# Kernel tuning notes

Measured on AMD Instinct MI355X. Metric: run time of the kernel, lower is better.

Reference implementation:

```python
import jax, jax.numpy as jnp
from jax import lax
import numpy as np

T, B, D = 1024, 2, 1024
E, TOP_K, ED, HD, MAXP = 12, 4, 256, 64, 64
H = ED // HD  # num_heads = 4


def setup_inputs() -> dict:
    rng = jax.random.key(0)
    ks = jax.random.split(rng, 9)
    s = 0.02
    return {
        "query": jax.random.normal(ks[0], (T, B, D), jnp.float32),
        "key": jax.random.normal(ks[1], (T, B, D), jnp.float32),
        "value": jax.random.normal(ks[2], (T, B, D), jnp.float32),
        "w_gate": jax.random.normal(ks[3], (D, E), jnp.float32) * s,
        "w_map": jax.random.normal(ks[4], (E, D, ED), jnp.float32) * s,
        "w_reduce": jax.random.normal(ks[5], (E, ED, D), jnp.float32) * s,
        "wk": jax.random.normal(ks[6], (D, ED), jnp.float32) * s,
        "wv": jax.random.normal(ks[7], (D, ED), jnp.float32) * s,
        "rel_pos_emb": jax.random.normal(ks[8], (H, HD, 2 * MAXP + 1), jnp.float32) * s,
    }


def reference(query, key, value, w_gate, w_map, w_reduce, wk, wv, rel_pos_emb):
    t, b, d = query.shape
    n = t * b
    scaling = HD ** (-0.25)

    # ---- MoE map (q projection): softmax gating, top-k dispatch ----
    x = query.reshape(n, d)
    probs = jax.nn.softmax(x @ w_gate, axis=-1)          # [N,E]
    gates, idx = lax.top_k(probs, TOP_K)                 # [N,K]
    all_map = jnp.einsum('nd,edh->neh', x, w_map)        # [N,E,ED]
    q = jnp.take_along_axis(all_map, idx[:, :, None], axis=1)  # [N,K,ED]

    # ---- dense k/v projections ----
    q = (q * scaling).reshape(t, b, TOP_K, H, HD).transpose(1, 2, 3, 0, 4)  # [B,K,H,T,HD]
    k = (key.reshape(n, d) @ wk * scaling).reshape(t, b, H, HD).transpose(1, 2, 0, 3)  # [B,H,S,HD]
    v = (value.reshape(n, d) @ wv).reshape(t, b, H, HD).transpose(1, 2, 0, 3)          # [B,H,S,HD]

    # ---- attention scores ----
    aw = jnp.einsum('bkhie,bhje->bkhij', q, k)           # [B,K,H,T,S]

    # ---- relative position logits (einsum + gather) ----
    s_len = t
    pos = jnp.arange(s_len)
    grid = jnp.clip(pos[None, :] - pos[:, None], 1 - MAXP, MAXP - 1) + MAXP  # [T,S]
    rel = jnp.einsum('bkhid,hdp->bkhip', q, rel_pos_emb)  # [B,K,H,T,2*MAXP+1]
    rel_g = rel[:, :, :, jnp.arange(t)[:, None], grid]    # [B,K,H,T,S]

    aw = jax.nn.softmax(aw + rel_g, axis=-1)
    attn = jnp.einsum('bkhij,bhje->bkhie', aw, v)         # [B,K,H,T,HD]

    # ---- MoE reduce (combine with gates) ----
    a = attn.transpose(3, 0, 1, 2, 4).reshape(n, TOP_K, ED)  # [N,K,ED]
    one_hot = jax.nn.one_hot(idx, E, dtype=a.dtype)          # [N,K,E]
    z = jnp.einsum('nkh,nke,nk->neh', a, one_hot, gates)     # [N,E,ED]
    out = jnp.einsum('neh,ehd->nd', z, w_reduce)             # [N,D]
    return out.reshape(t, b, d)
```

## Files before the change

kernel.cpp:

```cpp
#include <hip/hip_runtime.h>

#define T_    1024
#define B_    2
#define D_    1024
#define E_    12
#define TOPK  4
#define ED_   256
#define HD_   64
#define H_    4
#define N_    (T_*B_)
#define NROW  (N_*TOPK)
#define PB3_MAX 76
#define KA_   256

typedef __bf16 bf16x8 __attribute__((ext_vector_type(8)));
typedef _Float16 f16x8 __attribute__((ext_vector_type(8)));
typedef float  f32x4  __attribute__((ext_vector_type(4)));

__device__ __forceinline__ float sc_() { return 0.35355339059327373f; }

__device__ __forceinline__ void async16(const void* g, void* l) {
    __builtin_amdgcn_global_load_lds((const __attribute__((address_space(1))) void*)g,
                                     (__attribute__((address_space(3))) void*)l, 16, 0, 0);
}

__global__ void castwg_kernel(const float* __restrict__ wg, float* __restrict__ wgT) {
    int d = blockIdx.x * 256 + threadIdx.x;
#pragma unroll
    for (int e = 0; e < E_; ++e) wgT[e * D_ + d] = wg[d * E_ + e];
}

__global__ void __launch_bounds__(256)
gatecast_kernel(const float* __restrict__ x, const float* __restrict__ wgT,
                float* __restrict__ gates, int* __restrict__ idx,
                ushort* __restrict__ xb) {
    int w = threadIdx.x >> 6, L = threadIdx.x & 63;
    int n = blockIdx.x * 4 + w;
    const float* xr = x + (size_t)n * D_;
    float acc[E_];
#pragma unroll
    for (int e = 0; e < E_; ++e) acc[e] = 0.f;
#pragma unroll
    for (int it = 0; it < 4; ++it) {
        float4 xv = *(const float4*)(xr + it * 256 + L * 4);
        union { __bf16 h[4]; uint2 u; } pk;
        pk.h[0] = (__bf16)xv.x; pk.h[1] = (__bf16)xv.y;
        pk.h[2] = (__bf16)xv.z; pk.h[3] = (__bf16)xv.w;
        *(uint2*)(xb + (size_t)n * D_ + it * 256 + L * 4) = pk.u;
#pragma unroll
        for (int e = 0; e < E_; ++e) {
            float4 wv = *(const float4*)(wgT + e * D_ + it * 256 + L * 4);
            acc[e] += xv.x * wv.x + xv.y * wv.y + xv.z * wv.z + xv.w * wv.w;
        }
    }
#pragma unroll
    for (int e = 0; e < E_; ++e) {
        float v = acc[e];
        for (int o = 32; o > 0; o >>= 1) v += __shfl_down(v, o);
        acc[e] = v;
    }
    if (L == 0) {
        float mx = acc[0];
        for (int e = 1; e < E_; ++e) mx = fmaxf(mx, acc[e]);
        float s = 0.f, pr[E_];
        for (int e = 0; e < E_; ++e) { pr[e] = expf(acc[e] - mx); s += pr[e]; }
        float inv = 1.f / s;
        for (int e = 0; e < E_; ++e) pr[e] *= inv;
        for (int k = 0; k < TOPK; ++k) {
            int be = 0; float bv = -1.f;
            for (int e = 0; e < E_; ++e) if (pr[e] > bv) { bv = pr[e]; be = e; }
            gates[n * TOPK + k] = bv;
            idx[n * TOPK + k] = be;
            pr[be] = -1.f;
        }
    }
}

__global__ void hist_kernel(const int* __restrict__ idx, int* __restrict__ bcnt) {
    int b = blockIdx.x, tid = threadIdx.x, w = tid >> 6, L = tid & 63;
    int e = idx[b * 256 + tid];
    __shared__ int wcnt[4][E_];
#pragma unroll
    for (int e0 = 0; e0 < E_; ++e0) {
        unsigned long long m = __ballot(e == e0);
        if (L == 0) wcnt[w][e0] = (int)__popcll(m);
    }
    __syncthreads();
    if (tid < E_) bcnt[b * E_ + tid] = wcnt[0][tid] + wcnt[1][tid] + wcnt[2][tid] + wcnt[3][tid];
}

__global__ void scan_kernel(const int* __restrict__ bcnt, int* __restrict__ offs,
                            int* __restrict__ base,
                            int* __restrict__ rbe3, int* __restrict__ rbs3,
                            int* __restrict__ rbc3) {
    __shared__ int counts[E_], offl[E_ + 1];
    int tid = threadIdx.x;
    if (tid < E_) {
        int s = 0;
        for (int b = 0; b < 32; ++b) s += bcnt[b * E_ + tid];
        counts[tid] = s;
    }
    __syncthreads();
    if (tid == 0) {
        int o = 0;
        for (int e = 0; e < E_; ++e) { offl[e] = o; o += counts[e]; }
        offl[E_] = o;
    }
    __syncthreads();
    if (tid <= E_) offs[tid] = offl[tid];
    for (int i = tid; i < 32 * E_; i += 64) {
        int b = i / E_, e = i % E_;
        int run = offl[e];
        for (int bb = 0; bb < b; ++bb) run += bcnt[bb * E_ + e];
        base[i] = run;
    }
    if (tid < E_) {
        int pos = 0;
        for (int e = 0; e < tid; ++e) pos += (counts[e] + 127) >> 7;
        int c = counts[tid];
        for (int s = 0, k = 0; s < c; s += 128, ++k) {
            rbe3[pos + k] = tid; rbs3[pos + k] = offl[tid] + s;
            int rem = c - s; rbc3[pos + k] = rem < 128 ? rem : 128;
        }
    }
    int tot = 0;
    for (int e = 0; e < E_; ++e) tot += (counts[e] + 127) >> 7;
    for (int i = tot + tid; i < PB3_MAX; i += 64) {
        rbe3[i] = 0; rbs3[i] = 0; rbc3[i] = 0;
    }
}

__global__ void scatter_kernel(const int* __restrict__ idx, const int* __restrict__ base,
                               int* __restrict__ perm) {
    int b = blockIdx.x, tid = threadIdx.x, w = tid >> 6, L = tid & 63;
    int r = b * 256 + tid;
    int e = idx[r];
    __shared__ int wcnt[4][E_];
    int rankw = 0;
#pragma unroll
    for (int e0 = 0; e0 < E_; ++e0) {
        unsigned long long m = __ballot(e == e0);
        if (e == e0) rankw = (int)__popcll(m & ((1ULL << L) - 1ULL));
        if (L == 0) wcnt[w][e0] = (int)__popcll(m);
    }
    __syncthreads();
    int pre = 0;
    for (int w2 = 0; w2 < w; ++w2) pre += wcnt[w2][e];
    perm[base[b * E_ + e] + pre + rankw] = r;
}

__global__ void castkv2_kernel(const float* __restrict__ key, const float* __restrict__ value,
                               ushort* __restrict__ keyb, ushort* __restrict__ valb) {
    int g = blockIdx.x * 256 + threadIdx.x;
    int which = g >> 19, t = g & ((1 << 19) - 1);
    const float* src = which ? value : key;
    ushort* dst = which ? valb : keyb;
    float4 v = *(const float4*)(src + (size_t)t * 4);
    union { __bf16 h[4]; uint2 u; } pk;
    pk.h[0] = (__bf16)v.x; pk.h[1] = (__bf16)v.y;
    pk.h[2] = (__bf16)v.z; pk.h[3] = (__bf16)v.w;
    *(uint2*)(dst + (size_t)t * 4) = pk.u;
}

__global__ void castw_kernel(const float* __restrict__ wmap, ushort* __restrict__ wmapT) {
    int e = blockIdx.x, dt = blockIdx.y, et = blockIdx.z;
    __shared__ float ls[64][65];
    int c = threadIdx.x & 63, rg = threadIdx.x >> 6;
    const float* src = wmap + (size_t)e * (D_ * ED_) + (size_t)(dt * 64) * ED_ + et * 64;
#pragma unroll
    for (int q = 0; q < 16; ++q) {
        int r = q * 4 + rg;
        ls[r][c] = src[(size_t)r * ED_ + c];
    }
    __syncthreads();
    ushort* dst = wmapT + ((size_t)e << 18) + (size_t)(et * 64) * 1024 + dt * 64;
#pragma unroll
    for (int q = 0; q < 16; ++q) {
        int r = q * 4 + rg;
        union { __bf16 h; ushort u; } cv; cv.h = (__bf16)ls[c][r];
        dst[(size_t)r * 1024 + c] = cv.u;
    }
}

__global__ void castwkv_kernel(const float* __restrict__ wk, const float* __restrict__ wv,
                               ushort* __restrict__ wkT, ushort* __restrict__ wvT) {
    int which = blockIdx.x, dt = blockIdx.y, et = blockIdx.z;
    const float* w = which ? wv : wk;
    ushort* wT = which ? wvT : wkT;
    __shared__ float ls[64][65];
    int c = threadIdx.x & 63, rg = threadIdx.x >> 6;
    const float* src = w + (size_t)(dt * 64) * ED_ + et * 64;
#pragma unroll
    for (int q = 0; q < 16; ++q) {
        int r = q * 4 + rg;
        ls[r][c] = src[(size_t)r * ED_ + c];
    }
    __syncthreads();
    ushort* dst = wT + (size_t)(et * 64) * 1024 + dt * 64;
#pragma unroll
    for (int q = 0; q < 16; ++q) {
        int r = q * 4 + rg;
        union { __bf16 h; ushort u; } cv; cv.h = (__bf16)ls[c][r];
        dst[(size_t)r * 1024 + c] = cv.u;
    }
}

__global__ void castwred_kernel(const float* __restrict__ wred, ushort* __restrict__ wredf) {
    int e = blockIdx.x, et = blockIdx.y, dt = blockIdx.z;
    __shared__ float ls[64][65];
    int c = threadIdx.x & 63, rg = threadIdx.x >> 6;
    const float* src = wred + (size_t)e * (ED_ * D_) + (size_t)(et * 64) * D_ + dt * 64;
#pragma unroll
    for (int q = 0; q < 16; ++q) {
        int r = q * 4 + rg;
        ls[r][c] = src[(size_t)r * D_ + c];
    }
    __syncthreads();
    ushort* dst = wredf + (size_t)e * (D_ * KA_) + (size_t)(dt * 64) * KA_ + et * 64;
#pragma unroll
    for (int q = 0; q < 16; ++q) {
        int r = q * 4 + rg;
        union { _Float16 h; ushort u; } cv; cv.h = (_Float16)ls[c][r];
        dst[(size_t)r * KA_ + c] = cv.u;
    }
}

__global__ void castrpe_kernel(const float* __restrict__ rpe, ushort* __restrict__ rpeT) {
    int h = blockIdx.x;
    int p = threadIdx.x & 127;
    int dq = threadIdx.x >> 7;
#pragma unroll
    for (int d0 = 0; d0 < 64; d0 += 2) {
        int d = d0 + dq;
        union { __bf16 b; ushort u; } cv;
        cv.b = (__bf16)rpe[(size_t)(h * 64 + d) * 129 + p];
        rpeT[(size_t)(h * 128 + p) * 64 + d] = cv.u;
    }
}

__global__ void __launch_bounds__(256)
kv_mfma(const ushort* __restrict__ keyb, const ushort* __restrict__ valb,
        const ushort* __restrict__ wkT, const ushort* __restrict__ wvT,
        ushort* __restrict__ kpb, ushort* __restrict__ vpT) {
    int which = blockIdx.z;
    const ushort* xb = which ? valb : keyb;
    const ushort* wT = which ? wvT : wkT;
    int b = blockIdx.x >> 3, t0 = (blockIdx.x & 7) * 128;
    int n0 = blockIdx.y * 128;
    int tid = threadIdx.x, w = tid >> 6, L = tid & 63;
    __shared__ __align__(16) ushort As[2][128 * 64];
    __shared__ __align__(16) ushort Bs[2][128 * 64];

    int swz = ((L & 7) ^ ((L >> 3) & 7)) * 8;
    const ushort* asrc[4];
#pragma unroll
    for (int q = 0; q < 4; ++q) {
        int rl = q * 32 + w * 8 + (L >> 3);
        int an = (((t0 + rl) << 1) | b);
        asrc[q] = xb + (size_t)an * 1024 + swz;
    }
    const ushort* bsrc = wT + (size_t)(n0 + w * 8 + (L >> 3)) * 1024 + swz;

    f32x4 acc[2][8];
#pragma unroll
    for (int mt = 0; mt < 2; ++mt)
#pragma unroll
        for (int nt = 0; nt < 8; ++nt) acc[mt][nt] = (f32x4){0.f, 0.f, 0.f, 0.f};

    auto stage = [&](int kt, int bf) {
#pragma unroll
        for (int q = 0; q < 4; ++q)
            async16(asrc[q] + kt * 64, &As[bf][(q * 32 + w * 8) * 64]);
#pragma unroll
        for (int q = 0; q < 4; ++q)
            async16(bsrc + (size_t)(q * 32) * 1024 + kt * 64, &Bs[bf][(q * 32 + w * 8) * 64]);
    };
    auto compute = [&](int bf) {
        const ushort* AB = As[bf] + w * 32 * 64;
        const ushort* BB = Bs[bf];
#pragma unroll
        for (int ks = 0; ks < 2; ++ks) {
            int phys = (((ks * 4 + (L >> 4)) ^ (L & 7))) * 8;
            bf16x8 a0 = *(const bf16x8*)(AB + (L & 15) * 64 + phys);
            bf16x8 a1 = *(const bf16x8*)(AB + (16 + (L & 15)) * 64 + phys);
#pragma unroll
            for (int nt = 0; nt < 8; ++nt) {
                bf16x8 bfr = *(const bf16x8*)(BB + (nt * 16 + (L & 15)) * 64 + phys);
                acc[0][nt] = __builtin_amdgcn_mfma_f32_16x16x32_bf16(a0, bfr, acc[0][nt], 0, 0, 0);
                acc[1][nt] = __builtin_amdgcn_mfma_f32_16x16x32_bf16(a1, bfr, acc[1][nt], 0, 0, 0);
            }
        }
    };

    stage(0, 0);
    for (int t = 0; t < 16; ++t) {
        __syncthreads();
        if (t < 15) stage(t + 1, (t + 1) & 1);
        compute(t & 1);
    }

#pragma unroll
    for (int mt = 0; mt < 2; ++mt)
#pragma unroll
        for (int nt = 0; nt < 8; ++nt) {
            int ed = n0 + nt * 16 + (L & 15);
            int tb = t0 + w * 32 + mt * 16 + (L >> 4) * 4;
            if (which == 0) {
#pragma unroll
                for (int r = 0; r < 4; ++r) {
                    union { __bf16 h; ushort u; } cv;
                    cv.h = (__bf16)(acc[mt][nt][r] * sc_());
                    kpb[((size_t)((b << 10) + tb + r)) * ED_ + ed] = cv.u;
                }
            } else {
                int h = ed >> 6, d = ed & 63;
                union { __bf16 h4[4]; uint2 u; } pk;
#pragma unroll
                for (int r = 0; r < 4; ++r) pk.h4[r] = (__bf16)acc[mt][nt][r];
                *(uint2*)&vpT[((size_t)((b * 4 + h) * 64 + d)) * 1024 + tb] = pk.u;
            }
        }
}

__global__ void __launch_bounds__(256)
qproj_mfma(const ushort* __restrict__ xb, const ushort* __restrict__ wmapT,
           const int* __restrict__ perm,
           const int* __restrict__ rbe3, const int* __restrict__ rbs3,
           const int* __restrict__ rbc3,
           ushort* __restrict__ qpb) {
    int blk = blockIdx.x;
    int nr = rbc3[blk];
    if (nr == 0) return;
    int e = rbe3[blk], rs = rbs3[blk];
    int n0 = blockIdx.y * 128;
    int tid = threadIdx.x, w = tid >> 6, L = tid & 63;
    __shared__ __align__(16) ushort As[2][128 * 64];
    __shared__ __align__(16) ushort Bs[2][128 * 64];
    __shared__ int rows3[128];
    if (tid < 128) rows3[tid] = (tid < nr) ? perm[rs + tid] : -1;
    __syncthreads();

    int swz = ((L & 7) ^ ((L >> 3) & 7)) * 8;
    const ushort* asrc[4];
#pragma unroll
    for (int q = 0; q < 4; ++q) {
        int ar = rows3[q * 32 + w * 8 + (L >> 3)];
        asrc[q] = xb + (size_t)((ar < 0 ? 0 : ar) >> 2) * 1024 + swz;
    }
    const ushort* bsrc = wmapT + ((size_t)e << 18) + (size_t)(n0 + w * 8 + (L >> 3)) * 1024 + swz;

    f32x4 acc[2][8];
#pragma unroll
    for (int mt = 0; mt < 2; ++mt)
#pragma unroll
        for (int nt = 0; nt < 8; ++nt) acc[mt][nt] = (f32x4){0.f, 0.f, 0.f, 0.f};

    auto stage = [&](int kt, int bf) {
#pragma unroll
        for (int q = 0; q < 4; ++q)
            async16(asrc[q] + kt * 64, &As[bf][(q * 32 + w * 8) * 64]);
#pragma unroll
        for (int q = 0; q < 4; ++q)
            async16(bsrc + (size_t)(q * 32) * 1024 + kt * 64, &Bs[bf][(q * 32 + w * 8) * 64]);
    };
    auto compute = [&](int bf) {
        const ushort* AB = As[bf] + w * 32 * 64;
        const ushort* BB = Bs[bf];
#pragma unroll
        for (int ks = 0; ks < 2; ++ks) {
            int phys = (((ks * 4 + (L >> 4)) ^ (L & 7))) * 8;
            bf16x8 a0 = *(const bf16x8*)(AB + (L & 15) * 64 + phys);
            bf16x8 a1 = *(const bf16x8*)(AB + (16 + (L & 15)) * 64 + phys);
#pragma unroll
            for (int nt = 0; nt < 8; ++nt) {
                bf16x8 bfr = *(const bf16x8*)(BB + (nt * 16 + (L & 15)) * 64 + phys);
                acc[0][nt] = __builtin_amdgcn_mfma_f32_16x16x32_bf16(a0, bfr, acc[0][nt], 0, 0, 0);
                acc[1][nt] = __builtin_amdgcn_mfma_f32_16x16x32_bf16(a1, bfr, acc[1][nt], 0, 0, 0);
            }
        }
    };

    stage(0, 0);
    for (int t = 0; t < 16; ++t) {
        __syncthreads();
        if (t < 15) stage(t + 1, (t + 1) & 1);
        compute(t & 1);
    }

#pragma unroll
    for (int mt = 0; mt < 2; ++mt)
#pragma unroll
        for (int nt = 0; nt < 8; ++nt) {
            int n = n0 + nt * 16 + (L & 15);
#pragma unroll
            for (int r = 0; r < 4; ++r) {
                int m = w * 32 + mt * 16 + (L >> 4) * 4 + r;
                int rowg = rows3[m];
                if (rowg >= 0) {
                    union { __bf16 h; ushort u; } cv;
                    cv.h = (__bf16)(acc[mt][nt][r] * sc_());
                    qpb[(size_t)rowg * ED_ + n] = cv.u;
                }
            }
        }
}

__global__ void __launch_bounds__(256)
rel_mfma(const ushort* __restrict__ qpb, const ushort* __restrict__ rpeT,
         float* __restrict__ rel) {
    int m0 = blockIdx.x * 128;
    int h  = blockIdx.y;
    int tid = threadIdx.x, w = tid >> 6, L = tid & 63;
    __shared__ __align__(16) ushort As[128 * 64];
    __shared__ __align__(16) ushort Bs[128 * 64];

    int swz = ((L & 7) ^ ((L >> 3) & 7)) * 8;
    const ushort* asrc = qpb + (size_t)(m0 + w * 8 + (L >> 3)) * ED_ + h * HD_ + swz;
    const ushort* bsrc = rpeT + (size_t)(h * 128 + w * 8 + (L >> 3)) * 64 + swz;
#pragma unroll
    for (int q = 0; q < 4; ++q) {
        async16(asrc + (size_t)(q * 32) * ED_, &As[(q * 32 + w * 8) * 64]);
        async16(bsrc + (size_t)(q * 32) * 64,  &Bs[(q * 32 + w * 8) * 64]);
    }
    __syncthreads();

    f32x4 acc[2][8];
#pragma unroll
    for (int mt = 0; mt < 2; ++mt)
#pragma unroll
        for (int nt = 0; nt < 8; ++nt) acc[mt][nt] = (f32x4){0.f, 0.f, 0.f, 0.f};

    const ushort* AB = As + w * 32 * 64;
#pragma unroll
    for (int ks = 0; ks < 2; ++ks) {
        int phys = (((ks * 4 + (L >> 4)) ^ (L & 7))) * 8;
        bf16x8 a0 = *(const bf16x8*)(AB + (L & 15) * 64 + phys);
        bf16x8 a1 = *(const bf16x8*)(AB + (16 + (L & 15)) * 64 + phys);
#pragma unroll
        for (int nt = 0; nt < 8; ++nt) {
            bf16x8 b = *(const bf16x8*)(Bs + (nt * 16 + (L & 15)) * 64 + phys);
            acc[0][nt] = __builtin_amdgcn_mfma_f32_16x16x32_bf16(a0, b, acc[0][nt], 0, 0, 0);
            acc[1][nt] = __builtin_amdgcn_mfma_f32_16x16x32_bf16(a1, b, acc[1][nt], 0, 0, 0);
        }
    }

#pragma unroll
    for (int mt = 0; mt < 2; ++mt)
#pragma unroll
        for (int nt = 0; nt < 8; ++nt) {
            int p = nt * 16 + (L & 15);
#pragma unroll
            for (int r = 0; r < 4; ++r) {
                int qrow = m0 + w * 32 + mt * 16 + (L >> 4) * 4 + r;
                rel[((size_t)qrow * 4 + h) * 128 + p] = acc[mt][nt][r];
            }
        }
}

__global__ void __launch_bounds__(256)
attn_kernel(const ushort* __restrict__ qpb, const ushort* __restrict__ kpb,
            const ushort* __restrict__ vpT, const float* __restrict__ rel,
            const float* __restrict__ gates, ushort* __restrict__ az) {
    __shared__ __align__(16) ushort Ks[2][64 * 64];
    __shared__ __align__(16) ushort Vs[2][64 * 64];
    __shared__ __align__(16) ushort Ps[4][16 * 64];

    const int tid = threadIdx.x;
    const int w = tid >> 6, L = tid & 63;
    const int bkh = blockIdx.x & 31, it = blockIdx.x >> 5;
    const int h = bkh & 3, kk = (bkh >> 2) & 3, bb = bkh >> 4;
    const int i0w = it * 64 + w * 16;
    const int iL = i0w + (L & 15);
    const int row = ((iL * 2 + bb) << 2) | kk;

    const ushort* qrow = qpb + row * ED_ + h * HD_;
    bf16x8 qf0 = *(const bf16x8*)(qrow + (L >> 4) * 8);
    bf16x8 qf1 = *(const bf16x8*)(qrow + 32 + (L >> 4) * 8);

    const float* relrow = rel + ((size_t)row * 4 + h) * 128;
    float rel_lo = relrow[1], rel_hi = relrow[127];
    float gate = gates[row];

    f32x4 O[4];
#pragma unroll
    for (int mf = 0; mf < 4; ++mf) O[mf] = (f32x4){0.f, 0.f, 0.f, 0.f};
    float l_acc = 0.f;

    const ushort* ksrc = kpb + (size_t)(bb << 10) * ED_ + h * HD_;
    const ushort* vsrc = vpT + (size_t)((bb * 4 + h) * 64) * 1024;

    auto stage = [&](int t, int bf) {
        int j0 = t * 64;
#pragma unroll
        for (int q = 0; q < 2; ++q) {
            int r = L >> 3;
            int c = (L & 7) ^ r;
            const ushort* src = ksrc + (size_t)(j0 + w * 16 + q * 8 + r) * ED_ + c * 8;
            async16(src, &Ks[bf][(w * 16 + q * 8) * 64]);
        }
#pragma unroll
        for (int q = 0; q < 2; ++q) {
            int r = L >> 3;
            int d = w * 16 + q * 8 + r;
            int c = (L & 7) ^ (d & 7);
            const ushort* src = vsrc + (size_t)d * 1024 + j0 + c * 8;
            async16(src, &Vs[bf][(w * 16 + q * 8) * 64]);
        }
    };

    auto compute = [&](int bf, int j0) {
        const ushort* KB = Ks[bf];
        const ushort* VB = Vs[bf];
        ushort* PW = Ps[w];
#pragma unroll
        for (int jf = 0; jf < 4; ++jf) {
            int jrow = jf * 16 + (L & 15);
            bf16x8 a0 = *(const bf16x8*)(KB + jrow * 64 + (((L >> 4)) ^ (L & 7)) * 8);
            bf16x8 a1 = *(const bf16x8*)(KB + jrow * 64 + ((4 + (L >> 4)) ^ (L & 7)) * 8);
            f32x4 s = (f32x4){0.f, 0.f, 0.f, 0.f};
            s = __builtin_amdgcn_mfma_f32_16x16x32_bf16(a0, qf0, s, 0, 0, 0);
            s = __builtin_amdgcn_mfma_f32_16x16x32_bf16(a1, qf1, s, 0, 0, 0);
            int jlo = j0 + jf * 16;
            int jbase = jlo + (L >> 4) * 4;
            float pv[4];
            if (jlo >= i0w + 78) {
#pragma unroll
                for (int r = 0; r < 4; ++r) pv[r] = __expf(s[r] + rel_hi);
            } else if (jlo <= i0w - 78) {
#pragma unroll
                for (int r = 0; r < 4; ++r) pv[r] = __expf(s[r] + rel_lo);
            } else {
#pragma unroll
                for (int r = 0; r < 4; ++r) {
                    int dj = jbase + r - iL;
                    dj = dj < -63 ? -63 : (dj > 63 ? 63 : dj);
                    pv[r] = __expf(s[r] + relrow[dj + 64]);
                }
            }
            l_acc += (pv[0] + pv[1]) + (pv[2] + pv[3]);
            union { __bf16 h4[4]; uint2 u; } pk;
#pragma unroll
            for (int r = 0; r < 4; ++r) pk.h4[r] = (__bf16)pv[r];
            int iloc = L & 15;
            int chunk = jf * 2 + ((L >> 4) >> 1);
            int phys = chunk ^ (iloc & 7);
            *(uint2*)(PW + iloc * 64 + phys * 8 + ((L >> 4) & 1) * 4) = pk.u;
        }
#pragma unroll
        for (int ks = 0; ks < 2; ++ks) {
            int c = ks * 4 + (L >> 4);
            int phys = c ^ (L & 7);
            bf16x8 pf = *(const bf16x8*)(PW + (L & 15) * 64 + phys * 8);
#pragma unroll
            for (int mf = 0; mf < 4; ++mf) {
                bf16x8 vf = *(const bf16x8*)(VB + (mf * 16 + (L & 15)) * 64 + phys * 8);
                O[mf] = __builtin_amdgcn_mfma_f32_16x16x32_bf16(vf, pf, O[mf], 0, 0, 0);
            }
        }
    };

    stage(0, 0);
    for (int t = 0; t < 16; ++t) {
        __syncthreads();
        if (t < 15) stage(t + 1, (t + 1) & 1);
        compute(t & 1, t * 64);
    }

    l_acc += __shfl_xor(l_acc, 16);
    l_acc += __shfl_xor(l_acc, 32);
    float inv = gate / l_acc;
    ushort* azrow = az + (size_t)row * KA_ + h * HD_;
#pragma unroll
    for (int mf = 0; mf < 4; ++mf) {
        union { _Float16 h4[4]; uint2 u; } pk;
#pragma unroll
        for (int r = 0; r < 4; ++r) pk.h4[r] = (_Float16)(O[mf][r] * inv);
        int off = mf * 16 + (L >> 4) * 4;
        *(uint2*)(azrow + off) = pk.u;
    }
}

__global__ void zero_out(float* __restrict__ out) {
    int t = blockIdx.x * 256 + threadIdx.x;
    *(float4*)(out + (size_t)t * 4) = make_float4(0.f, 0.f, 0.f, 0.f);
}

__global__ void __launch_bounds__(256)
reduce_mfma(const ushort* __restrict__ az, const ushort* __restrict__ wredf,
            const int* __restrict__ perm,
            const int* __restrict__ rbe3, const int* __restrict__ rbs3,
            const int* __restrict__ rbc3, float* __restrict__ out) {
    int blk = blockIdx.x;
    int nr = rbc3[blk];
    if (nr == 0) return;
    int e = rbe3[blk], rs = rbs3[blk];
    int n0 = blockIdx.y * 128;
    int tid = threadIdx.x, w = tid >> 6, L = tid & 63;
    __shared__ __align__(16) ushort As[2][128 * 64];
    __shared__ __align__(16) ushort Bs[2][128 * 64];
    __shared__ int rows3[128];
    if (tid < 128) rows3[tid] = (tid < nr) ? perm[rs + tid] : -1;
    __syncthreads();

    int swz = ((L & 7) ^ ((L >> 3) & 7)) * 8;
    const ushort* asrc[4];
#pragma unroll
    for (int q = 0; q < 4; ++q) {
        int ar = rows3[q * 32 + w * 8 + (L >> 3)];
        asrc[q] = az + (size_t)(ar < 0 ? 0 : ar) * KA_ + swz;
    }
    const ushort* bsrc = wredf + (size_t)e * (D_ * KA_)
                       + (size_t)(n0 + w * 8 + (L >> 3)) * KA_ + swz;

    f32x4 acc[2][8];
#pragma unroll
    for (int mt = 0; mt < 2; ++mt)
#pragma unroll
// ... 34 lines not shown
#pragma unroll
    for (int mt = 0; mt < 2; ++mt)
#pragma unroll
        for (int nt = 0; nt < 8; ++nt) {
            int n = n0 + nt * 16 + (L & 15);
#pragma unroll
            for (int r = 0; r < 4; ++r) {
                int m = w * 32 + mt * 16 + (L >> 4) * 4 + r;
                int rowg = rows3[m];
                if (rowg >= 0)
                    unsafeAtomicAdd(out + (size_t)(rowg >> 2) * D_ + n, acc[mt][nt][r]);
            }
        }
}

extern "C" void kernel_launch(void* const* d_in, const int* in_sizes, int n_in,
                              void* d_out, int out_size, void* d_ws, size_t ws_size,
                              hipStream_t stream) {
    const float* query = (const float*)d_in[0];
    const float* key   = (const float*)d_in[1];
    const float* value = (const float*)d_in[2];
    const float* wg    = (const float*)d_in[3];
    const float* wmap  = (const float*)d_in[4];
    const float* wred  = (const float*)d_in[5];
    const float* wk    = (const float*)d_in[6];
    const float* wv    = (const float*)d_in[7];
    const float* rpe   = (const float*)d_in[8];
    float* out = (float*)d_out;

    char* ws = (char*)d_ws;
    float*  gates = (float*)(ws + 0);
    int*    idx   = (int*)(ws + (32 << 10));
    char*   misc  = ws + (64 << 10);
    int*    offs   = (int*)(misc + 128);
    int*    bcnt   = (int*)(misc + 1024);
    int*    base   = (int*)(misc + 3072);
    int*    rbe3   = (int*)(misc + 12288);
    int*    rbs3   = (int*)(misc + 12800);
    int*    rbc3   = (int*)(misc + 13312);
    int*    perm  = (int*)(ws + (96 << 10));
    char*   base_ = ws + (128 << 10);
    ushort* rpeT  = (ushort*)(base_);
    ushort* qpb   = (ushort*)(base_ + (8u  << 20));
    ushort* kpb   = (ushort*)(base_ + (12u << 20));
    ushort* vpT   = (ushort*)(base_ + (13u << 20));
    ushort* xb    = (ushort*)(base_ + (14u << 20));
    ushort* wmapT = (ushort*)(base_ + (18u << 20));
    ushort* keyb  = (ushort*)(base_ + (24u << 20));
    ushort* valb  = (ushort*)(base_ + (28u << 20));
    ushort* wkT   = (ushort*)(base_ + (32u << 20));
    ushort* wvT   = (ushort*)(base_ + (32u << 20) + (512u << 10));
    ushort* az    = (ushort*)(base_ + (48u << 20));
    ushort* wredf = (ushort*)(base_ + (61u << 20));
    float*  rel   = (float*)(base_ + (80u << 20));
    float*  wgT   = (float*)(base_ + (96u << 20));

    zero_out<<<(N_ * D_) / 1024, 256, 0, stream>>>(out);
    castwg_kernel<<<D_ / 256, 256, 0, stream>>>(wg, wgT);
    castkv2_kernel<<<(2 * N_ * D_) / 1024, 256, 0, stream>>>(key, value, keyb, valb);
    castw_kernel<<<dim3(E_, 16, 4), 256, 0, stream>>>(wmap, wmapT);
    castwkv_kernel<<<dim3(2, 16, 4), 256, 0, stream>>>(wk, wv, wkT, wvT);
    castwred_kernel<<<dim3(E_, 4, 16), 256, 0, stream>>>(wred, wredf);
    castrpe_kernel<<<dim3(H_), 256, 0, stream>>>(rpe, rpeT);
    gatecast_kernel<<<N_ / 4, 256, 0, stream>>>(query, wgT, gates, idx, xb);
    hist_kernel<<<NROW / 256, 256, 0, stream>>>(idx, bcnt);
    scan_kernel<<<1, 64, 0, stream>>>(bcnt, offs, base, rbe3, rbs3, rbc3);
    scatter_kernel<<<NROW / 256, 256, 0, stream>>>(idx, base, perm);
    kv_mfma<<<dim3(16, 2, 2), 256, 0, stream>>>(keyb, valb, wkT, wvT, kpb, vpT);
    qproj_mfma<<<dim3(PB3_MAX, 2), 256, 0, stream>>>(xb, wmapT, perm, rbe3, rbs3, rbc3, qpb);
    rel_mfma<<<dim3(64, 4), 256, 0, stream>>>(qpb, rpeT, rel);
    attn_kernel<<<512, 256, 0, stream>>>(qpb, kpb, vpT, rel, gates, az);
    reduce_mfma<<<dim3(PB3_MAX, 8), 256, 0, stream>>>(az, wredf, perm, rbe3, rbs3, rbc3, out);
}
```

Before: 257.0 us.

## Fuse prep kernels, merge routing passes, combine projections, store rel logits in fp16

Folds the zeroing, weight-cast, kv-cast, gating and rpe-transpose kernels into one block-indexed prep kernel, with the gate weights transposed into shared memory. Replaces the hist, scan and scatter passes with a single 1024-thread routing kernel. Merges the k/v and MoE q projections into one launch. Stores the relative-position logits as fp16 to halve their traffic into attention. The aim is to cut launch count and serialization overhead, in exchange for a single-block routing kernel and fp16 precision loss on the rel logits.

Result: faster. 220.6 us (-14.1%).

```diff
diff --git a/kernel.cpp b/kernel.cpp
--- a/kernel.cpp
+++ b/kernel.cpp
@@ -24,80 +24,178 @@
                                      (__attribute__((address_space(3))) void*)l, 16, 0, 0);
 }
 
-__global__ void castwg_kernel(const float* __restrict__ wg, float* __restrict__ wgT) {
-    int d = blockIdx.x * 256 + threadIdx.x;
-#pragma unroll
-    for (int e = 0; e < E_; ++e) wgT[e * D_ + d] = wg[d * E_ + e];
-}
-
+#define PREP_GRID 8324
 __global__ void __launch_bounds__(256)
-gatecast_kernel(const float* __restrict__ x, const float* __restrict__ wgT,
-                float* __restrict__ gates, int* __restrict__ idx,
-                ushort* __restrict__ xb) {
-    int w = threadIdx.x >> 6, L = threadIdx.x & 63;
-    int n = blockIdx.x * 4 + w;
-    const float* xr = x + (size_t)n * D_;
-    float acc[E_];
-#pragma unroll
-    for (int e = 0; e < E_; ++e) acc[e] = 0.f;
-#pragma unroll
-    for (int it = 0; it < 4; ++it) {
-        float4 xv = *(const float4*)(xr + it * 256 + L * 4);
+prep_kernel(const float* __restrict__ query, const float* __restrict__ key,
+            const float* __restrict__ value, const float* __restrict__ wg,
+            const float* __restrict__ wmap, const float* __restrict__ wred,
+            const float* __restrict__ wk, const float* __restrict__ wv,
+            const float* __restrict__ rpe,
+            float* __restrict__ gates, int* __restrict__ idx, ushort* __restrict__ xb,
+            ushort* __restrict__ keyb, ushort* __restrict__ valb,
+            ushort* __restrict__ wmapT, ushort* __restrict__ wredf,
+            ushort* __restrict__ wkT, ushort* __restrict__ wvT,
+            ushort* __restrict__ rpeT, float* __restrict__ out) {
+    __shared__ __align__(16) float lsbuf[12288];
+    int bid = blockIdx.x, tid = threadIdx.x;
+
+    if (bid < 512) {
+        float (*lsw)[1024] = (float(*)[1024])lsbuf;
+        for (int i = tid; i < 12288; i += 256) {
+            int d = i / 12, e = i - d * 12;
+            lsw[e][d] = wg[i];
+        }
+        __syncthreads();
+        int w = tid >> 6, L = tid & 63;
+        int n = bid * 4 + w;
+        const float* xr = query + (size_t)n * D_;
+        float acc[E_];
+#pragma unroll
+        for (int e = 0; e < E_; ++e) acc[e] = 0.f;
+#pragma unroll
+        for (int it = 0; it < 4; ++it) {
+            float4 xv = *(const float4*)(xr + it * 256 + L * 4);
+            union { __bf16 h[4]; uint2 u; } pk;
+            pk.h[0] = (__bf16)xv.x; pk.h[1] = (__bf16)xv.y;
+            pk.h[2] = (__bf16)xv.z; pk.h[3] = (__bf16)xv.w;
+            *(uint2*)(xb + (size_t)n * D_ + it * 256 + L * 4) = pk.u;
+#pragma unroll
+            for (int e = 0; e < E_; ++e) {
+                float4 wvv = *(const float4*)(&lsw[e][it * 256 + L * 4]);
+                acc[e] += xv.x * wvv.x + xv.y * wvv.y + xv.z * wvv.z + xv.w * wvv.w;
+            }
+        }
+#pragma unroll
+        for (int e = 0; e < E_; ++e) {
+            float v = acc[e];
+            for (int o = 32; o > 0; o >>= 1) v += __shfl_down(v, o);
+            acc[e] = v;
+        }
+        if (L == 0) {
+            float mx = acc[0];
+            for (int e = 1; e < E_; ++e) mx = fmaxf(mx, acc[e]);
+            float s = 0.f, pr[E_];
+            for (int e = 0; e < E_; ++e) { pr[e] = expf(acc[e] - mx); s += pr[e]; }
+            float inv = 1.f / s;
+            for (int e = 0; e < E_; ++e) pr[e] *= inv;
+            for (int k = 0; k < TOPK; ++k) {
+                int be = 0; float bv = -1.f;
+                for (int e = 0; e < E_; ++e) if (pr[e] > bv) { bv = pr[e]; be = e; }
+                gates[n * TOPK + k] = bv;
+                idx[n * TOPK + k] = be;
+                pr[be] = -1.f;
+            }
+        }
+    } else if (bid < 1280) {
+        float (*ls)[65] = (float(*)[65])lsbuf;
+        int i = bid - 512;
+        int e = i >> 6, rem = i & 63, et = rem >> 4, dt = rem & 15;
+        int c = tid & 63, rg = tid >> 6;
+        const float* src = wred + (size_t)e * (ED_ * D_) + (size_t)(et * 64) * D_ + dt * 64;
+#pragma unroll
+        for (int q = 0; q < 16; ++q) {
+            int r = q * 4 + rg;
+            ls[r][c] = src[(size_t)r * D_ + c];
+        }
+        __syncthreads();
+        ushort* dst = wredf + (size_t)e * (D_ * KA_) + (size_t)(dt * 64) * KA_ + et * 64;
+#pragma unroll
+        for (int q = 0; q < 16; ++q) {
+            int r = q * 4 + rg;
+            union { _Float16 h; ushort u; } cv; cv.h = (_Float16)ls[c][r];
+            dst[(size_t)r * KA_ + c] = cv.u;
+        }
+    } else if (bid < 5376) {
+        int g = (bid - 1280) * 256 + tid;
+        int which = g >> 19, t = g & ((1 << 19) - 1);
+        const float* src = which ? value : key;
+        ushort* dst = which ? valb : keyb;
+        float4 v = *(const float4*)(src + (size_t)t * 4);
         union { __bf16 h[4]; uint2 u; } pk;
-        pk.h[0] = (__bf16)xv.x; pk.h[1] = (__bf16)xv.y;
-        pk.h[2] = (__bf16)xv.z; pk.h[3] = (__bf16)xv.w;
-        *(uint2*)(xb + (size_t)n * D_ + it * 256 + L * 4) = pk.u;
-#pragma unroll
-        for (int e = 0; e < E_; ++e) {
-            float4 wv = *(const float4*)(wgT + e * D_ + it * 256 + L * 4);
-            acc[e] += xv.x * wv.x + xv.y * wv.y + xv.z * wv.z + xv.w * wv.w;
-        }
-    }
-#pragma unroll
-    for (int e = 0; e < E_; ++e) {
-        float v = acc[e];
-        for (int o = 32; o > 0; o >>= 1) v += __shfl_down(v, o);
-        acc[e] = v;
-    }
-    if (L == 0) {
-        float mx = acc[0];
-        for (int e = 1; e < E_; ++e) mx = fmaxf(mx, acc[e]);
-        float s = 0.f, pr[E_];
-        for (int e = 0; e < E_; ++e) { pr[e] = expf(acc[e] - mx); s += pr[e]; }
-        float inv = 1.f / s;
-        for (int e = 0; e < E_; ++e) pr[e] *= inv;
-        for (int k = 0; k < TOPK; ++k) {
-            int be = 0; float bv = -1.f;
-            for (int e = 0; e < E_; ++e) if (pr[e] > bv) { bv = pr[e]; be = e; }
-            gates[n * TOPK + k] = bv;
-            idx[n * TOPK + k] = be;
-            pr[be] = -1.f;
-        }
-    }
-}
-
-__global__ void hist_kernel(const int* __restrict__ idx, int* __restrict__ bcnt) {
-    int b = blockIdx.x, tid = threadIdx.x, w = tid >> 6, L = tid & 63;
-    int e = idx[b * 256 + tid];
-    __shared__ int wcnt[4][E_];
-#pragma unroll
-    for (int e0 = 0; e0 < E_; ++e0) {
-        unsigned long long m = __ballot(e == e0);
-        if (L == 0) wcnt[w][e0] = (int)__popcll(m);
+        pk.h[0] = (__bf16)v.x; pk.h[1] = (__bf16)v.y;
+        pk.h[2] = (__bf16)v.z; pk.h[3] = (__bf16)v.w;
+        *(uint2*)(dst + (size_t)t * 4) = pk.u;
+    } else if (bid < 6144) {
+        float (*ls)[65] = (float(*)[65])lsbuf;
+        int i = bid - 5376;
+        int e = i >> 6, rem = i & 63, dt = rem >> 2, et = rem & 3;
+        int c = tid & 63, rg = tid >> 6;
+        const float* src = wmap + (size_t)e * (D_ * ED_) + (size_t)(dt * 64) * ED_ + et * 64;
+#pragma unroll
+        for (int q = 0; q < 16; ++q) {
+            int r = q * 4 + rg;
+            ls[r][c] = src[(size_t)r * ED_ + c];
+        }
+        __syncthreads();
+        ushort* dst = wmapT + ((size_t)e << 18) + (size_t)(et * 64) * 1024 + dt * 64;
+#pragma unroll
+        for (int q = 0; q < 16; ++q) {
+            int r = q * 4 + rg;
+            union { __bf16 h; ushort u; } cv; cv.h = (__bf16)ls[c][r];
+            dst[(size_t)r * 1024 + c] = cv.u;
+        }
+    } else if (bid < 8192) {
+        int t = (bid - 6144) * 256 + tid;
+        *(float4*)(out + (size_t)t * 4) = make_float4(0.f, 0.f, 0.f, 0.f);
+    } else if (bid < 8320) {
+        float (*ls)[65] = (float(*)[65])lsbuf;
+        int i = bid - 8192;
+        int which = i >> 6, rem = i & 63, dt = rem >> 2, et = rem & 3;
+        const float* w = which ? wv : wk;
+        ushort* wT = which ? wvT : wkT;
+        int c = tid & 63, rg = tid >> 6;
+        const float* src = w + (size_t)(dt * 64) * ED_ + et * 64;
+#pragma unroll
+        for (int q = 0; q < 16; ++q) {
+            int r = q * 4 + rg;
+            ls[r][c] = src[(size_t)r * ED_ + c];
+        }
+        __syncthreads();
+        ushort* dst = wT + (size_t)(et * 64) * 1024 + dt * 64;
+#pragma unroll
+        for (int q = 0; q < 16; ++q) {
+            int r = q * 4 + rg;
+            union { __bf16 h; ushort u; } cv; cv.h = (__bf16)ls[c][r];
+            dst[(size_t)r * 1024 + c] = cv.u;
+        }
+    } else {
+        int h = bid - 8320;
+        int p = tid & 127, dq = tid >> 7;
+#pragma unroll
+        for (int d0 = 0; d0 < 64; d0 += 2) {
+            int d = d0 + dq;
+            union { __bf16 b; ushort u; } cv;
+            cv.b = (__bf16)rpe[(size_t)(h * 64 + d) * 129 + p];
+            rpeT[(size_t)(h * 128 + p) * 64 + d] = cv.u;
+        }
+    }
+}
+
+__global__ void __launch_bounds__(1024)
+hss_kernel(const int* __restrict__ idx,
+           int* __restrict__ rbe3, int* __restrict__ rbs3, int* __restrict__ rbc3,
+           int* __restrict__ perm) {
+    __shared__ int cnt[128][E_];
+    __shared__ int pref[128][E_];
+    __shared__ int offl[E_ + 1];
+    __shared__ int counts[E_];
+    int tid = threadIdx.x, w = tid >> 6, L = tid & 63;
+    int mye[8];
+#pragma unroll
+    for (int g = 0; g < 8; ++g) {
+        int c = w * 8 + g;
+        int e = idx[c * 64 + L];
+        mye[g] = e;
+#pragma unroll
+        for (int e0 = 0; e0 < E_; ++e0) {
+            unsigned long long m = __ballot(e == e0);
+            if (L == 0) cnt[c][e0] = (int)__popcll(m);
+        }
     }
     __syncthreads();
-    if (tid < E_) bcnt[b * E_ + tid] = wcnt[0][tid] + wcnt[1][tid] + wcnt[2][tid] + wcnt[3][tid];
-}
-
-__global__ void scan_kernel(const int* __restrict__ bcnt, int* __restrict__ offs,
-                            int* __restrict__ base,
-                            int* __restrict__ rbe3, int* __restrict__ rbs3,
-                            int* __restrict__ rbc3) {
-    __shared__ int counts[E_], offl[E_ + 1];
-    int tid = threadIdx.x;
     if (tid < E_) {
         int s = 0;
-        for (int b = 0; b < 32; ++b) s += bcnt[b * E_ + tid];
+        for (int c = 0; c < 128; ++c) { pref[c][tid] = s; s += cnt[c][tid]; }
         counts[tid] = s;
     }
     __syncthreads();
@@ -107,166 +205,38 @@
         offl[E_] = o;
     }
     __syncthreads();
-    if (tid <= E_) offs[tid] = offl[tid];
-    for (int i = tid; i < 32 * E_; i += 64) {
-        int b = i / E_, e = i % E_;
-        int run = offl[e];
-        for (int bb = 0; bb < b; ++bb) run += bcnt[bb * E_ + e];
-        base[i] = run;
-    }
     if (tid < E_) {
         int pos = 0;
         for (int e = 0; e < tid; ++e) pos += (counts[e] + 127) >> 7;
-        int c = counts[tid];
-        for (int s = 0, k = 0; s < c; s += 128, ++k) {
+        int c0 = counts[tid];
+        for (int s = 0, k = 0; s < c0; s += 128, ++k) {
             rbe3[pos + k] = tid; rbs3[pos + k] = offl[tid] + s;
-            int rem = c - s; rbc3[pos + k] = rem < 128 ? rem : 128;
+            int rem = c0 - s; rbc3[pos + k] = rem < 128 ? rem : 128;
         }
     }
     int tot = 0;
     for (int e = 0; e < E_; ++e) tot += (counts[e] + 127) >> 7;
-    for (int i = tot + tid; i < PB3_MAX; i += 64) {
+    for (int i = tot + tid; i < PB3_MAX; i += 1024) {
         rbe3[i] = 0; rbs3[i] = 0; rbc3[i] = 0;
     }
-}
-
-__global__ void scatter_kernel(const int* __restrict__ idx, const int* __restrict__ base,
-                               int* __restrict__ perm) {
-    int b = blockIdx.x, tid = threadIdx.x, w = tid >> 6, L = tid & 63;
-    int r = b * 256 + tid;
-    int e = idx[r];
-    __shared__ int wcnt[4][E_];
-    int rankw = 0;
-#pragma unroll
-    for (int e0 = 0; e0 < E_; ++e0) {
-        unsigned long long m = __ballot(e == e0);
-        if (e == e0) rankw = (int)__popcll(m & ((1ULL << L) - 1ULL));
-        if (L == 0) wcnt[w][e0] = (int)__popcll(m);
-    }
-    __syncthreads();
-    int pre = 0;
-    for (int w2 = 0; w2 < w; ++w2) pre += wcnt[w2][e];
-    perm[base[b * E_ + e] + pre + rankw] = r;
-}
-
-__global__ void castkv2_kernel(const float* __restrict__ key, const float* __restrict__ value,
-                               ushort* __restrict__ keyb, ushort* __restrict__ valb) {
-    int g = blockIdx.x * 256 + threadIdx.x;
-    int which = g >> 19, t = g & ((1 << 19) - 1);
-    const float* src = which ? value : key;
-    ushort* dst = which ? valb : keyb;
-    float4 v = *(const float4*)(src + (size_t)t * 4);
-    union { __bf16 h[4]; uint2 u; } pk;
-    pk.h[0] = (__bf16)v.x; pk.h[1] = (__bf16)v.y;
-    pk.h[2] = (__bf16)v.z; pk.h[3] = (__bf16)v.w;
-    *(uint2*)(dst + (size_t)t * 4) = pk.u;
-}
-
-__global__ void castw_kernel(const float* __restrict__ wmap, ushort* __restrict__ wmapT) {
-    int e = blockIdx.x, dt = blockIdx.y, et = blockIdx.z;
-    __shared__ float ls[64][65];
-    int c = threadIdx.x & 63, rg = threadIdx.x >> 6;
-    const float* src = wmap + (size_t)e * (D_ * ED_) + (size_t)(dt * 64) * ED_ + et * 64;
-#pragma unroll
-    for (int q = 0; q < 16; ++q) {
-        int r = q * 4 + rg;
-        ls[r][c] = src[(size_t)r * ED_ + c];
-    }
-    __syncthreads();
-    ushort* dst = wmapT + ((size_t)e << 18) + (size_t)(et * 64) * 1024 + dt * 64;
-#pragma unroll
-    for (int q = 0; q < 16; ++q) {
-        int r = q * 4 + rg;
-        union { __bf16 h; ushort u; } cv; cv.h = (__bf16)ls[c][r];
-        dst[(size_t)r * 1024 + c] = cv.u;
-    }
-}
-
-__global__ void castwkv_kernel(const float* __restrict__ wk, const float* __restrict__ wv,
-                               ushort* __restrict__ wkT, ushort* __restrict__ wvT) {
-    int which = blockIdx.x, dt = blockIdx.y, et = blockIdx.z;
-    const float* w = which ? wv : wk;
-    ushort* wT = which ? wvT : wkT;
-    __shared__ float ls[64][65];
-    int c = threadIdx.x & 63, rg = threadIdx.x >> 6;
-    const float* src = w + (size_t)(dt * 64) * ED_ + et * 64;
-#pragma unroll
-    for (int q = 0; q < 16; ++q) {
-        int r = q * 4 + rg;
-        ls[r][c] = src[(size_t)r * ED_ + c];
-    }
-    __syncthreads();
-    ushort* dst = wT + (size_t)(et * 64) * 1024 + dt * 64;
-#pragma unroll
-    for (int q = 0; q < 16; ++q) {
-        int r = q * 4 + rg;
-        union { __bf16 h; ushort u; } cv; cv.h = (__bf16)ls[c][r];
-        dst[(size_t)r * 1024 + c] = cv.u;
-    }
-}
-
-__global__ void castwred_kernel(const float* __restrict__ wred, ushort* __restrict__ wredf) {
-    int e = blockIdx.x, et = blockIdx.y, dt = blockIdx.z;
-    __shared__ float ls[64][65];
-    int c = threadIdx.x & 63, rg = threadIdx.x >> 6;
-    const float* src = wred + (size_t)e * (ED_ * D_) + (size_t)(et * 64) * D_ + dt * 64;
-#pragma unroll
-    for (int q = 0; q < 16; ++q) {
-        int r = q * 4 + rg;
-        ls[r][c] = src[(size_t)r * D_ + c];
-    }
-    __syncthreads();
-    ushort* dst = wredf + (size_t)e * (D_ * KA_) + (size_t)(dt * 64) * KA_ + et * 64;
-#pragma unroll
-    for (int q = 0; q < 16; ++q) {
-        int r = q * 4 + rg;
-        union { _Float16 h; ushort u; } cv; cv.h = (_Float16)ls[c][r];
-        dst[(size_t)r * KA_ + c] = cv.u;
-    }
-}
-
-__global__ void castrpe_kernel(const float* __restrict__ rpe, ushort* __restrict__ rpeT) {
-    int h = blockIdx.x;
-    int p = threadIdx.x & 127;
-    int dq = threadIdx.x >> 7;
-#pragma unroll
-    for (int d0 = 0; d0 < 64; d0 += 2) {
-        int d = d0 + dq;
-        union { __bf16 b; ushort u; } cv;
-        cv.b = (__bf16)rpe[(size_t)(h * 64 + d) * 129 + p];
-        rpeT[(size_t)(h * 128 + p) * 64 + d] = cv.u;
-    }
-}
-
-__global__ void __launch_bounds__(256)
-kv_mfma(const ushort* __restrict__ keyb, const ushort* __restrict__ valb,
-        const ushort* __restrict__ wkT, const ushort* __restrict__ wvT,
-        ushort* __restrict__ kpb, ushort* __restrict__ vpT) {
-    int which = blockIdx.z;
-    const ushort* xb = which ? valb : keyb;
-    const ushort* wT = which ? wvT : wkT;
-    int b = blockIdx.x >> 3, t0 = (blockIdx.x & 7) * 128;
-    int n0 = blockIdx.y * 128;
-    int tid = threadIdx.x, w = tid >> 6, L = tid & 63;
-    __shared__ __align__(16) ushort As[2][128 * 64];
-    __shared__ __align__(16) ushort Bs[2][128 * 64];
-
-    int swz = ((L & 7) ^ ((L >> 3) & 7)) * 8;
-    const ushort* asrc[4];
-#pragma unroll
-    for (int q = 0; q < 4; ++q) {
-        int rl = q * 32 + w * 8 + (L >> 3);
-        int an = (((t0 + rl) << 1) | b);
-        asrc[q] = xb + (size_t)an * 1024 + swz;
-    }
-    const ushort* bsrc = wT + (size_t)(n0 + w * 8 + (L >> 3)) * 1024 + swz;
-
-    f32x4 acc[2][8];
-#pragma unroll
-    for (int mt = 0; mt < 2; ++mt)
-#pragma unroll
-        for (int nt = 0; nt < 8; ++nt) acc[mt][nt] = (f32x4){0.f, 0.f, 0.f, 0.f};
-
+#pragma unroll
+    for (int g = 0; g < 8; ++g) {
+        int c = w * 8 + g;
+        int e = mye[g];
+        int rank = 0;
+#pragma unroll
+        for (int e0 = 0; e0 < E_; ++e0) {
+            unsigned long long m = __ballot(e == e0);
+            if (e == e0) rank = (int)__popcll(m & ((1ULL << L) - 1ULL));
+        }
+        perm[offl[e] + pref[c][e] + rank] = c * 64 + L;
+    }
+}
+
+__device__ __forceinline__ void mfma_k16_bf16(
+    const ushort* const asrc[4], const ushort* bsrc,
+    ushort As[2][128 * 64], ushort Bs[2][128 * 64],
+    f32x4 acc[2][8], int w, int L) {
     auto stage = [&](int kt, int bf) {
 #pragma unroll
         for (int q = 0; q < 4; ++q)
@@ -291,63 +261,28 @@
             }
         }
     };
-
     stage(0, 0);
     for (int t = 0; t < 16; ++t) {
         __syncthreads();
         if (t < 15) stage(t + 1, (t + 1) & 1);
         compute(t & 1);
     }
-
-#pragma unroll
-    for (int mt = 0; mt < 2; ++mt)
-#pragma unroll
-        for (int nt = 0; nt < 8; ++nt) {
-            int ed = n0 + nt * 16 + (L & 15);
-            int tb = t0 + w * 32 + mt * 16 + (L >> 4) * 4;
-            if (which == 0) {
-#pragma unroll
-                for (int r = 0; r < 4; ++r) {
-                    union { __bf16 h; ushort u; } cv;
-                    cv.h = (__bf16)(acc[mt][nt][r] * sc_());
-                    kpb[((size_t)((b << 10) + tb + r)) * ED_ + ed] = cv.u;
-                }
-            } else {
-                int h = ed >> 6, d = ed & 63;
-                union { __bf16 h4[4]; uint2 u; } pk;
-#pragma unroll
-                for (int r = 0; r < 4; ++r) pk.h4[r] = (__bf16)acc[mt][nt][r];
-                *(uint2*)&vpT[((size_t)((b * 4 + h) * 64 + d)) * 1024 + tb] = pk.u;
-            }
-        }
 }
 
 __global__ void __launch_bounds__(256)
-qproj_mfma(const ushort* __restrict__ xb, const ushort* __restrict__ wmapT,
-           const int* __restrict__ perm,
-           const int* __restrict__ rbe3, const int* __restrict__ rbs3,
-           const int* __restrict__ rbc3,
-           ushort* __restrict__ qpb) {
-    int blk = blockIdx.x;
-    int nr = rbc3[blk];
-    if (nr == 0) return;
-    int e = rbe3[blk], rs = rbs3[blk];
-    int n0 = blockIdx.y * 128;
-    int tid = threadIdx.x, w = tid >> 6, L = tid & 63;
+proj_mfma(const ushort* __restrict__ keyb, const ushort* __restrict__ valb,
+          const ushort* __restrict__ wkT, const ushort* __restrict__ wvT,
+          const ushort* __restrict__ xb, const ushort* __restrict__ wmapT,
+          const int* __restrict__ perm,
+          const int* __restrict__ rbe3, const int* __restrict__ rbs3,
+          const int* __restrict__ rbc3,
+          ushort* __restrict__ kpb, ushort* __restrict__ vpT,
+          ushort* __restrict__ qpb) {
     __shared__ __align__(16) ushort As[2][128 * 64];
     __shared__ __align__(16) ushort Bs[2][128 * 64];
     __shared__ int rows3[128];
-    if (tid < 128) rows3[tid] = (tid < nr) ? perm[rs + tid] : -1;
-    __syncthreads();
-
+    int tid = threadIdx.x, w = tid >> 6, L = tid & 63;
     int swz = ((L & 7) ^ ((L >> 3) & 7)) * 8;
-    const ushort* asrc[4];
-#pragma unroll
-    for (int q = 0; q < 4; ++q) {
-        int ar = rows3[q * 32 + w * 8 + (L >> 3)];
-        asrc[q] = xb + (size_t)((ar < 0 ? 0 : ar) >> 2) * 1024 + swz;
-    }
-    const ushort* bsrc = wmapT + ((size_t)e << 18) + (size_t)(n0 + w * 8 + (L >> 3)) * 1024 + swz;
 
     f32x4 acc[2][8];
 #pragma unroll
@@ -355,59 +290,88 @@
 #pragma unroll
         for (int nt = 0; nt < 8; ++nt) acc[mt][nt] = (f32x4){0.f, 0.f, 0.f, 0.f};
 
-    auto stage = [&](int kt, int bf) {
-#pragma unroll
-        for (int q = 0; q < 4; ++q)
-            async16(asrc[q] + kt * 64, &As[bf][(q * 32 + w * 8) * 64]);
-#pragma unroll
-        for (int q = 0; q < 4; ++q)
-            async16(bsrc + (size_t)(q * 32) * 1024 + kt * 64, &Bs[bf][(q * 32 + w * 8) * 64]);
-    };
-    auto compute = [&](int bf) {
-        const ushort* AB = As[bf] + w * 32 * 64;
-        const ushort* BB = Bs[bf];
-#pragma unroll
-        for (int ks = 0; ks < 2; ++ks) {
-            int phys = (((ks * 4 + (L >> 4)) ^ (L & 7))) * 8;
-            bf16x8 a0 = *(const bf16x8*)(AB + (L & 15) * 64 + phys);
-            bf16x8 a1 = *(const bf16x8*)(AB + (16 + (L & 15)) * 64 + phys);
+    if (blockIdx.x < 64) {
+        int which = blockIdx.x >> 5;
+        int n0 = ((blockIdx.x >> 4) & 1) * 128;
+        int mc = blockIdx.x & 15;
+        int b = mc >> 3, t0 = (mc & 7) * 128;
+        const ushort* xsrc = which ? valb : keyb;
+        const ushort* wT = which ? wvT : wkT;
+        const ushort* asrc[4];
+#pragma unroll
+        for (int q = 0; q < 4; ++q) {
+            int rl = q * 32 + w * 8 + (L >> 3);
+            int an = (((t0 + rl) << 1) | b);
+            asrc[q] = xsrc + (size_t)an * 1024 + swz;
+        }
+        const ushort* bsrc = wT + (size_t)(n0 + w * 8 + (L >> 3)) * 1024 + swz;
+
+        mfma_k16_bf16(asrc, bsrc, As, Bs, acc, w, L);
+
+#pragma unroll
+        for (int mt = 0; mt < 2; ++mt)
 #pragma unroll
             for (int nt = 0; nt < 8; ++nt) {
-                bf16x8 bfr = *(const bf16x8*)(BB + (nt * 16 + (L & 15)) * 64 + phys);
-                acc[0][nt] = __builtin_amdgcn_mfma_f32_16x16x32_bf16(a0, bfr, acc[0][nt], 0, 0, 0);
-                acc[1][nt] = __builtin_amdgcn_mfma_f32_16x16x32_bf16(a1, bfr, acc[1][nt], 0, 0, 0);
-            }
-        }
-    };
-
-    stage(0, 0);
-    for (int t = 0; t < 16; ++t) {
-        __syncthreads();
-        if (t < 15) stage(t + 1, (t + 1) & 1);
-        compute(t & 1);
-    }
-
-#pragma unroll
-    for (int mt = 0; mt < 2; ++mt)
-#pragma unroll
-        for (int nt = 0; nt < 8; ++nt) {
-            int n = n0 + nt * 16 + (L & 15);
-#pragma unroll
-            for (int r = 0; r < 4; ++r) {
-                int m = w * 32 + mt * 16 + (L >> 4) * 4 + r;
-                int rowg = rows3[m];
-                if (rowg >= 0) {
-                    union { __bf16 h; ushort u; } cv;
-                    cv.h = (__bf16)(acc[mt][nt][r] * sc_());
-                    qpb[(size_t)rowg * ED_ + n] = cv.u;
+                int ed = n0 + nt * 16 + (L & 15);
+                int tb = t0 + w * 32 + mt * 16 + (L >> 4) * 4;
+                if (which == 0) {
+#pragma unroll
+                    for (int r = 0; r < 4; ++r) {
+                        union { __bf16 h; ushort u; } cv;
+                        cv.h = (__bf16)(acc[mt][nt][r] * sc_());
+                        kpb[((size_t)((b << 10) + tb + r)) * ED_ + ed] = cv.u;
+                    }
+                } else {
+                    int h = ed >> 6, d = ed & 63;
+                    union { __bf16 h4[4]; uint2 u; } pk;
+#pragma unroll
+                    for (int r = 0; r < 4; ++r) pk.h4[r] = (__bf16)acc[mt][nt][r];
+                    *(uint2*)&vpT[((size_t)((b * 4 + h) * 64 + d)) * 1024 + tb] = pk.u;
                 }
             }
-        }
+    } else {
+        int qid = blockIdx.x - 64;
+        int blk = qid >> 1;
+        int n0 = (qid & 1) * 128;
+        int nr = rbc3[blk];
+        if (nr == 0) return;
+        int e = rbe3[blk], rs = rbs3[blk];
+        if (tid < 128) rows3[tid] = (tid < nr) ? perm[rs + tid] : -1;
+        __syncthreads();
+
+        const ushort* asrc[4];
+#pragma unroll
+        for (int q = 0; q < 4; ++q) {
+            int ar = rows3[q * 32 + w * 8 + (L >> 3)];
+            asrc[q] = xb + (size_t)((ar < 0 ? 0 : ar) >> 2) * 1024 + swz;
+        }
+        const ushort* bsrc = wmapT + ((size_t)e << 18)
+                           + (size_t)(n0 + w * 8 + (L >> 3)) * 1024 + swz;
+
+        mfma_k16_bf16(asrc, bsrc, As, Bs, acc, w, L);
+
+#pragma unroll
+        for (int mt = 0; mt < 2; ++mt)
+#pragma unroll
+            for (int nt = 0; nt < 8; ++nt) {
+                int n = n0 + nt * 16 + (L & 15);
+#pragma unroll
+                for (int r = 0; r < 4; ++r) {
+                    int m = w * 32 + mt * 16 + (L >> 4) * 4 + r;
+                    int rowg = rows3[m];
+                    if (rowg >= 0) {
+                        union { __bf16 h; ushort u; } cv;
+                        cv.h = (__bf16)(acc[mt][nt][r] * sc_());
+                        qpb[(size_t)rowg * ED_ + n] = cv.u;
+                    }
+                }
+            }
+    }
 }
 
 __global__ void __launch_bounds__(256)
 rel_mfma(const ushort* __restrict__ qpb, const ushort* __restrict__ rpeT,
-         float* __restrict__ rel) {
+         ushort* __restrict__ relh) {
     int m0 = blockIdx.x * 128;
     int h  = blockIdx.y;
     int tid = threadIdx.x, w = tid >> 6, L = tid & 63;
@@ -452,14 +416,16 @@
 #pragma unroll
             for (int r = 0; r < 4; ++r) {
                 int qrow = m0 + w * 32 + mt * 16 + (L >> 4) * 4 + r;
-                rel[((size_t)qrow * 4 + h) * 128 + p] = acc[mt][nt][r];
+                union { _Float16 h16; ushort u; } cv;
+                cv.h16 = (_Float16)acc[mt][nt][r];
+                relh[((size_t)qrow * 4 + h) * 128 + p] = cv.u;
             }
         }
 }
 
 __global__ void __launch_bounds__(256)
 attn_kernel(const ushort* __restrict__ qpb, const ushort* __restrict__ kpb,
-            const ushort* __restrict__ vpT, const float* __restrict__ rel,
+            const ushort* __restrict__ vpT, const ushort* __restrict__ relh,
             const float* __restrict__ gates, ushort* __restrict__ az) {
     __shared__ __align__(16) ushort Ks[2][64 * 64];
     __shared__ __align__(16) ushort Vs[2][64 * 64];
@@ -477,8 +443,9 @@
     bf16x8 qf0 = *(const bf16x8*)(qrow + (L >> 4) * 8);
     bf16x8 qf1 = *(const bf16x8*)(qrow + 32 + (L >> 4) * 8);
 
-    const float* relrow = rel + ((size_t)row * 4 + h) * 128;
-    float rel_lo = relrow[1], rel_hi = relrow[127];
+    const ushort* relrow = relh + ((size_t)row * 4 + h) * 128;
+    float rel_lo = (float)*(const _Float16*)(relrow + 1);
+    float rel_hi = (float)*(const _Float16*)(relrow + 127);
     float gate = gates[row];
 
     f32x4 O[4];
@@ -534,7 +501,7 @@
                 for (int r = 0; r < 4; ++r) {
                     int dj = jbase + r - iL;
                     dj = dj < -63 ? -63 : (dj > 63 ? 63 : dj);
-                    pv[r] = __expf(s[r] + relrow[dj + 64]);
+                    pv[r] = __expf(s[r] + (float)*(const _Float16*)(relrow + dj + 64));
                 }
             }
             l_acc += (pv[0] + pv[1]) + (pv[2] + pv[3]);
@@ -578,11 +545,6 @@
         int off = mf * 16 + (L >> 4) * 4;
         *(uint2*)(azrow + off) = pk.u;
     }
-}
-
-__global__ void zero_out(float* __restrict__ out) {
-    int t = blockIdx.x * 256 + threadIdx.x;
-    *(float4*)(out + (size_t)t * 4) = make_float4(0.f, 0.f, 0.f, 0.f);
 }
 
 __global__ void __launch_bounds__(256)
@@ -683,9 +645,6 @@
     float*  gates = (float*)(ws + 0);
     int*    idx   = (int*)(ws + (32 << 10));
     char*   misc  = ws + (64 << 10);
-    int*    offs   = (int*)(misc + 128);
-    int*    bcnt   = (int*)(misc + 1024);
-    int*    base   = (int*)(misc + 3072);
     int*    rbe3   = (int*)(misc + 12288);
     int*    rbs3   = (int*)(misc + 12800);
     int*    rbc3   = (int*)(misc + 13312);
@@ -703,23 +662,14 @@
     ushort* wvT   = (ushort*)(base_ + (32u << 20) + (512u << 10));
     ushort* az    = (ushort*)(base_ + (48u << 20));
     ushort* wredf = (ushort*)(base_ + (61u << 20));
-    float*  rel   = (float*)(base_ + (80u << 20));
-    float*  wgT   = (float*)(base_ + (96u << 20));
-
-    zero_out<<<(N_ * D_) / 1024, 256, 0, stream>>>(out);
-    castwg_kernel<<<D_ / 256, 256, 0, stream>>>(wg, wgT);
-    castkv2_kernel<<<(2 * N_ * D_) / 1024, 256, 0, stream>>>(key, value, keyb, valb);
-    castw_kernel<<<dim3(E_, 16, 4), 256, 0, stream>>>(wmap, wmapT);
-    castwkv_kernel<<<dim3(2, 16, 4), 256, 0, stream>>>(wk, wv, wkT, wvT);
-    castwred_kernel<<<dim3(E_, 4, 16), 256, 0, stream>>>(wred, wredf);
-    castrpe_kernel<<<dim3(H_), 256, 0, stream>>>(rpe, rpeT);
-    gatecast_kernel<<<N_ / 4, 256, 0, stream>>>(query, wgT, gates, idx, xb);
-    hist_kernel<<<NROW / 256, 256, 0, stream>>>(idx, bcnt);
-    scan_kernel<<<1, 64, 0, stream>>>(bcnt, offs, base, rbe3, rbs3, rbc3);
-    scatter_kernel<<<NROW / 256, 256, 0, stream>>>(idx, base, perm);
-    kv_mfma<<<dim3(16, 2, 2), 256, 0, stream>>>(keyb, valb, wkT, wvT, kpb, vpT);
-    qproj_mfma<<<dim3(PB3_MAX, 2), 256, 0, stream>>>(xb, wmapT, perm, rbe3, rbs3, rbc3, qpb);
-    rel_mfma<<<dim3(64, 4), 256, 0, stream>>>(qpb, rpeT, rel);
-    attn_kernel<<<512, 256, 0, stream>>>(qpb, kpb, vpT, rel, gates, az);
+    ushort* relh  = (ushort*)(base_ + (80u << 20));
+
+    prep_kernel<<<PREP_GRID, 256, 0, stream>>>(query, key, value, wg, wmap, wred,
+        wk, wv, rpe, gates, idx, xb, keyb, valb, wmapT, wredf, wkT, wvT, rpeT, out);
+    hss_kernel<<<1, 1024, 0, stream>>>(idx, rbe3, rbs3, rbc3, perm);
+    proj_mfma<<<64 + 2 * PB3_MAX, 256, 0, stream>>>(keyb, valb, wkT, wvT, xb, wmapT,
+        perm, rbe3, rbs3, rbc3, kpb, vpT, qpb);
+    rel_mfma<<<dim3(64, 4), 256, 0, stream>>>(qpb, rpeT, relh);
+    attn_kernel<<<512, 256, 0, stream>>>(qpb, kpb, vpT, relh, gates, az);
     reduce_mfma<<<dim3(PB3_MAX, 8), 256, 0, stream>>>(az, wredf, perm, rbe3, rbs3, rbc3, out);
 }
```
